# Optimization experiments

Hardware: AMD Instinct MI355X
Metric: run time of the kernel (lower is better)

The kernel has to match this reference:

```python
import jax, jax.numpy as jnp
import numpy as np

N_ENC, B, T, D_ENC = 3, 256, 168, 32
U, H, D_DEC, D_EXT = 256, 24, 1, 16


def _gru_cell(x, h, W, Uw, b):
    # Keras-style GRU cell: gates ordered [z, r, n]; h' = (1-z)*h + z*n
    u = Uw.shape[0]
    xg = x @ W + b            # [B, 3U]
    hg = h @ Uw               # [B, 3U]
    z = jax.nn.sigmoid(xg[:, :u] + hg[:, :u])
    r = jax.nn.sigmoid(xg[:, u:2 * u] + hg[:, u:2 * u])
    n = jnp.tanh(xg[:, 2 * u:] + r * hg[:, 2 * u:])
    return (1.0 - z) * h + z * n


def _run_gru(x, W, Uw, b):
    # x: [B, T, D] -> outputs [B, T, U], last state [B, U]
    h0 = jnp.zeros((x.shape[0], Uw.shape[0]), x.dtype)

    def step(h, xt):
        h2 = _gru_cell(xt, h, W, Uw, b)
        return h2, h2

    hT, ys = jax.lax.scan(step, h0, jnp.swapaxes(x, 0, 1))
    return jnp.swapaxes(ys, 0, 1), hT


def setup_inputs() -> dict:
    key = jax.random.key(0)
    ks = jax.random.split(key, 18)
    s = 0.05
    d_in_dec = N_ENC * U + D_DEC
    d_state = U + N_ENC * U
    return {
        "enc_inputs": jax.random.normal(ks[0], (N_ENC, B, T, D_ENC), jnp.float32),
        "dec_input": jax.random.normal(ks[1], (B, H, D_DEC), jnp.float32),
        "ext_feat": jax.random.normal(ks[2], (B, H, D_EXT), jnp.float32),
        "enc_W": jax.random.normal(ks[3], (N_ENC, D_ENC, 3 * U), jnp.float32) * s,
        "enc_U": jax.random.normal(ks[4], (N_ENC, U, 3 * U), jnp.float32) * s,
        "enc_b": jnp.zeros((N_ENC, 3 * U), jnp.float32),
        "att_W1": jax.random.normal(ks[5], (N_ENC, U, U), jnp.float32) * s,
        "att_W2": jax.random.normal(ks[6], (N_ENC, U, U), jnp.float32) * s,
        "att_v": jax.random.normal(ks[7], (N_ENC, U), jnp.float32) * s,
        "dec_W": jax.random.normal(ks[8], (d_in_dec, 3 * U), jnp.float32) * s,
        "dec_U": jax.random.normal(ks[9], (U, 3 * U), jnp.float32) * s,
        "dec_b": jnp.zeros((3 * U,), jnp.float32),
        "ext_W": jax.random.normal(ks[10], (D_EXT, U), jnp.float32) * s,
        "ext_b": jnp.zeros((U,), jnp.float32),
        "out1_W": jax.random.normal(ks[11], (d_state + U, U), jnp.float32) * s,
        "out1_b": jnp.zeros((U,), jnp.float32),
        "out2_W": jax.random.normal(ks[12], (U, D_DEC), jnp.float32) * s,
        "out2_b": jnp.zeros((D_DEC,), jnp.float32),
    }


def reference(enc_inputs, dec_input, ext_feat, enc_W, enc_U, enc_b,
              att_W1, att_W2, att_v, dec_W, dec_U, dec_b,
              ext_W, ext_b, out1_W, out1_b, out2_W, out2_b):
    b = dec_input.shape[0]
    horizon = dec_input.shape[1]

    # ---- encoders (vmapped GRU over the n_enc streams) ----
    enc_out, _ = jax.vmap(_run_gru)(enc_inputs, enc_W, enc_U, enc_b)  # [n,B,T,U]
    # Precompute Bahdanau keys once: W1 @ enc_outputs
    enc_proj = jnp.einsum('nbtu,nuv->nbtv', enc_out, att_W1)          # [n,B,T,U]

    h0 = jnp.zeros((b, U), dec_input.dtype)
    c0 = jnp.zeros((b, N_ENC * U), dec_input.dtype)

    def dec_step(carry, d_t):
        h, c = carry
        x_t = jnp.concatenate([c, d_t], axis=-1)                      # [B, n*U + D_dec]
        h = _gru_cell(x_t, h, dec_W, dec_U, dec_b)                    # [B, U]
        # Bahdanau attention per encoder, query = decoder state
        q = jnp.einsum('bu,nuv->nbv', h, att_W2)                      # [n,B,U]
        score = jnp.einsum('nbtv,nv->nbt',
                           jnp.tanh(enc_proj + q[:, :, None, :]), att_v)
        alpha = jax.nn.softmax(score, axis=-1)                        # [n,B,T]
        ctx = jnp.einsum('nbt,nbtu->nbu', alpha, enc_out)             # [n,B,U]
        c = jnp.transpose(ctx, (1, 0, 2)).reshape(b, N_ENC * U)
        return (h, c), h

    (h_last, c_last), _ = jax.lax.scan(dec_step, (h0, c0),
                                       jnp.swapaxes(dec_input, 0, 1))

    # ---- output head ----
    state = jnp.concatenate([h_last, c_last], axis=-1)                # [B, U + n*U]
    ed = jnp.broadcast_to(state[:, None, :], (b, horizon, state.shape[-1]))
    ext = jax.nn.relu(ext_feat @ ext_W + ext_b)                       # [B, H, U]
    x = jnp.concatenate([ed, ext], axis=-1)
    x = jax.nn.relu(x @ out1_W + out1_b)
    return x @ out2_W + out2_b                                        # [B, H, target_dim]
```

## Files before the change

kernel.cpp:

```cpp
#include <hip/hip_runtime.h>
#include <math.h>

typedef unsigned short u16;
typedef float f4v __attribute__((ext_vector_type(4)));
typedef _Float16 hfv8 __attribute__((ext_vector_type(8)));

#define MFMAH(a,b,c) __builtin_amdgcn_mfma_f32_16x16x32_f16((a),(b),(c),0,0,0)

__device__ __forceinline__ float bf2f(u16 x){
    unsigned int u = ((unsigned int)x) << 16;
    float f; __builtin_memcpy(&f, &u, 4); return f;
}
__device__ __forceinline__ u16 f2bf(float f){
    unsigned int u; __builtin_memcpy(&u, &f, 4);
    u += 0x7fffu + ((u >> 16) & 1u);
    return (u16)(u >> 16);
}
__device__ __forceinline__ u16 f2h(float f){
    _Float16 h = (_Float16)f;
    u16 b; __builtin_memcpy(&b, &h, 2); return b;
}
__device__ __forceinline__ float h2f(u16 b){
    _Float16 h; __builtin_memcpy(&h, &b, 2); return (float)h;
}
__device__ __forceinline__ float ldmix(const void* p, long i, int mode){
    if (mode) return ((const float*)p)[i];
    return bf2f(((const u16*)p)[i]);
}
__device__ __forceinline__ float frcp(float x){ return __builtin_amdgcn_rcpf(x); }
__device__ __forceinline__ float sigf(float x){ return frcp(1.0f+__expf(-x)); }
__device__ __forceinline__ float tanh_fast(float x){
    float e = __expf(2.0f*x);
    return 1.0f - 2.0f*frcp(1.0f+e);
}

#define BATCH 256
#define TLEN 168
#define HOR 24

#define OFF_FLAG 0ull
#define OFF_SENT 16ull
#define OFF_CNT  128ull
#define OFF_WF   256ull
#define OFF_UP   8721920ull
#define OFF_WP   9901568ull
#define OFF_DWP  10049024ull
#define OFF_DUP  11228672ull
#define OFF_H0   11621888ull
#define OFF_H1   11884032ull
#define OFF_C    12146176ull
#define OFF_W1P  12932608ull
#define OFF_SP   13719040ull
#define OFF_E    13981184ull
#define OFF_PACK0 OFF_E
#define OFF_PACK1 (OFF_E + 524288ull)
#define OFF_W2P   (OFF_E + 1048576ull)
#define OFF_ENCOUT 17126912ull
#define OFF_PROJ 83187200ull
#define NEED_BYTES 149247488ull

#define W_ENCW 0
#define W_ENCU 73728
#define W_ENCB 663552
#define W_AW1  665856
#define W_AW2  862464
#define W_AV   1059072
#define W_DECW 1059840
#define W_DECU 1650432
#define W_DECB 1847040
#define W_EXTW 1847808
#define W_EXTB 1851904
#define W_O1W  1852160
#define W_O1B  2179840
#define W_O2W  2180096
#define W_O2B  2180352

__device__ const int c_wsz[15]  = {73728,589824,2304,196608,196608,768,590592,196608,768,4096,256,327680,256,256,1};
__device__ const int c_woff[15] = {W_ENCW,W_ENCU,W_ENCB,W_AW1,W_AW2,W_AV,W_DECW,W_DECU,W_DECB,W_EXTW,W_EXTB,W_O1W,W_O1B,W_O2W,W_O2B};

struct P15 { const void* p[15]; };

#define SENT_MAGIC 0x5AFE0000u
__device__ __forceinline__ void put_sent(char* ws, int idx){
    ((unsigned int*)(ws+OFF_SENT))[idx] = SENT_MAGIC | (unsigned int)idx;
}

__global__ __launch_bounds__(256) void k_probe(const u16* w16, char* ws)
{
    __shared__ float red[256];
    int tid = threadIdx.x;
    float mb = 0.0f;
    for (int i = tid; i < 2048; i += 256){
        float a = fabsf(bf2f(w16[i]));
        if (a > mb) mb = a;
    }
    red[tid] = mb;
    __syncthreads();
    if (tid == 0){
        for (int i = 1; i < 256; ++i) if (red[i] > mb) mb = red[i];
        *(int*)(ws+OFF_FLAG) = (mb > 1000.0f) ? 1 : 0;
        put_sent(ws, 0);
    }
}

__global__ __launch_bounds__(256) void k_convert(P15 in, char* ws)
{
    int mode = *(const int*)(ws+OFF_FLAG);
    float* F = (float*)(ws+OFF_WF);
    int y = blockIdx.y;
    int sz = c_wsz[y], off = c_woff[y];
    for (long i = (long)blockIdx.x*256 + threadIdx.x; i < sz; i += 256L*256L)
        F[off + i] = ldmix(in.p[y], i, mode);
    if (blockIdx.x==0 && blockIdx.y==0 && threadIdx.x==0) put_sent(ws, 1);
}

__global__ __launch_bounds__(64) void k_pack(char* ws)
{
    const float* F = (const float*)(ws+OFF_WF);
    int m = blockIdx.y;
    if (m >= 11){
        const float* s = F + W_AW2 + (m-11)*65536;
        u16* d = (u16*)(ws+OFF_W2P) + (m-11)*65536;
        int i = blockIdx.x*64 + threadIdx.x;
        if (i < 65536){
            int k = i>>8, u = i&255;
            d[(k>>1)*512 + u*2 + (k&1)] = f2h(s[i]);
        }
        return;
    }
    const float* src; u16* dst; int K, N; int duo = 0;
    switch (m) {
      case 0: case 1: case 2:
        src = F + W_ENCU + m*196608; dst = (u16*)(ws+OFF_UP) + m*196608; K=256; N=768; break;
      case 3: case 4: case 5:
        src = F + W_ENCW + (m-3)*24576; dst = (u16*)(ws+OFF_WP) + (m-3)*24576; K=32; N=768; break;
      case 6:
        src = F + W_DECW; dst = (u16*)(ws+OFF_DWP); K=768; N=768; break;
      case 7:
        src = F + W_DECU; dst = (u16*)(ws+OFF_DUP); K=256; N=768; break;
      default:
        src = F + W_AW1 + (m-8)*65536; dst = (u16*)(ws+OFF_W1P) + (m-8)*131072; K=256; N=256; duo=1; break;
    }
    int KT = K>>5, NT = N>>4;
    int tau = blockIdx.x;
    if (tau < KT*NT){
        int ct = tau / KT, kt = tau % KT;
        int l = threadIdx.x, q = l>>4, c = l&15;
        #pragma unroll
        for (int j = 0; j < 8; ++j){
            float v = src[(size_t)(kt*32 + q*8 + j)*N + ct*16 + c];
            u16 hi = f2h(v);
            size_t di = ((size_t)(ct*KT+kt)*64 + l)*8 + j;
            dst[di] = hi;
            if (duo) dst[65536 + di] = f2h(v - h2f(hi));
        }
    }
    if (blockIdx.x==0 && blockIdx.y==0 && threadIdx.x==0) put_sent(ws, 6);
}

__global__ __launch_bounds__(256) void k_init(char* ws)
{
    long idx = (long)blockIdx.x*256 + threadIdx.x;
    if (idx < 65536) ((float*)(ws+OFF_H0))[idx] = 0.0f;
    else if (idx < 262144) ((float*)(ws+OFF_C))[idx-65536] = 0.0f;
    else if (idx < 393216) ((int*)(ws+OFF_PACK0))[idx-262144] = 0;
    if (idx < 32) ((unsigned*)(ws+OFF_CNT))[idx] = 0u;
}

__global__ __launch_bounds__(512, 2) void k_enc(const void* __restrict__ enc_in,
                                                char* __restrict__ ws,
                                                u16* __restrict__ enc_out)
{
    const float* __restrict__ F = (const float*)(ws+OFF_WF);
    int mode = *(const int*)(ws+OFF_FLAG);
    const int n  = blockIdx.y;
    const int b0 = blockIdx.x*16;
    const int tid = threadIdx.x;
    const int w = tid>>6, l = tid&63, quad = l>>4, c15 = l&15;

    __shared__ __align__(16) u16 hA[2][8][64][8];
    __shared__ __align__(16) u16 sx[2][64][8];
    __shared__ __align__(16) u16 nU[128][64][8];

    const u16* __restrict__ upn = (const u16*)(ws+OFF_UP) + n*196608;
    const u16* __restrict__ wpn = (const u16*)(ws+OFF_WP) + n*24576;

    {
        const uint4* s4 = (const uint4*)(upn + 131072);
        uint4* d4 = (uint4*)&nU[0][0][0];
        for (int i = tid; i < 8192; i += 512) d4[i] = s4[i];
    }
    {
        int* z0 = (int*)&hA[0][0][0][0];
        for (int i = tid; i < 2048; i += 512) z0[i]=0;
    }
    float h[8];
    #pragma unroll
    for (int i=0;i<8;++i) h[i]=0.0f;

    float bzr[2], brr[2], bnr[2];
    #pragma unroll
    for (int si=0;si<2;++si){
        int u = (w*2+si)*16 + c15;
        bzr[si] = F[W_ENCB + n*768 + u];
        brr[si] = F[W_ENCB + n*768 + 256 + u];
        bnr[si] = F[W_ENCB + n*768 + 512 + u];
    }

    hfv8 Bz[2][8], Br[2][8];
    #pragma unroll
    for (int si=0;si<2;++si){
        int ct = w*2+si;
        #pragma unroll
        for (int kt=0;kt<8;++kt){
            Bz[si][kt] = *(const hfv8*)(upn + ((size_t)(ct*8+kt)*64 + l)*8);
            Br[si][kt] = *(const hfv8*)(upn + ((size_t)((16+ct)*8+kt)*64 + l)*8);
        }
    }
    #pragma unroll
    for (int si=0;si<2;++si)
        #pragma unroll
        for (int kt=0;kt<8;++kt)
            asm volatile("" : "+v"(Bz[si][kt]), "+v"(Br[si][kt]));

    const int mm = tid>>5, kk2 = tid&31;
    sx[0][(kk2>>3)*16 + mm][kk2&7] =
        f2h(ldmix(enc_in, (((long)(n*BATCH + b0 + mm))*TLEN + 0)*32 + kk2, mode));
    __syncthreads();

    for (int t = 0; t < TLEN; ++t){
        int p = t & 1;
        int tt = (t+1 < TLEN) ? (t+1) : t;
        float xr = ldmix(enc_in, (((long)(n*BATCH + b0 + mm))*TLEN + tt)*32 + kk2, mode);

        hfv8 ah[8];
        #pragma unroll
        for (int kt=0; kt<8; ++kt)
            ah[kt] = *(const hfv8*)&hA[p][kt][l][0];
        hfv8 ax = *(const hfv8*)&sx[p][l][0];

        #pragma unroll
        for (int si=0; si<2; ++si){
            int ct = w*2 + si;
            f4v az  = {0.f,0.f,0.f,0.f};
            f4v ar  = {0.f,0.f,0.f,0.f};
            f4v anx = {0.f,0.f,0.f,0.f};
            f4v anh = {0.f,0.f,0.f,0.f};
            az  = MFMAH(ax, *(const hfv8*)(wpn + ((size_t)ct*64 + l)*8), az);
            ar  = MFMAH(ax, *(const hfv8*)(wpn + ((size_t)(16+ct)*64 + l)*8), ar);
            anx = MFMAH(ax, *(const hfv8*)(wpn + ((size_t)(32+ct)*64 + l)*8), anx);
            #pragma unroll
            for (int kt=0; kt<8; ++kt) az = MFMAH(ah[kt], Bz[si][kt], az);
            #pragma unroll
            for (int kt=0; kt<8; ++kt) ar = MFMAH(ah[kt], Br[si][kt], ar);
            #pragma unroll
            for (int kt=0; kt<8; ++kt)
                anh = MFMAH(ah[kt], *(const hfv8*)&nU[ct*8+kt][l][0], anh);
            int u = ct*16 + c15;
            #pragma unroll
            for (int j=0;j<4;++j){
                int m = quad*4 + j;
                float z = sigf(az[j] + bzr[si]);
                float r = sigf(ar[j] + brr[si]);
                float ng = tanh_fast(anx[j] + bnr[si] + r*anh[j]);
                float hn = (1.0f - z)*h[si*4+j] + z*ng;
                h[si*4+j] = hn;
                int kt = u>>5, q2 = (u>>3)&3, j2 = u&7;
                hA[1-p][kt][q2*16+m][j2] = f2h(hn);
            }
        }
        sx[1-p][(kk2>>3)*16 + mm][kk2&7] = f2h(xr);
        __syncthreads();
        {
            int c = tid & 31, m2 = tid >> 5;
            *reinterpret_cast<uint4*>(enc_out + (((long)(n*BATCH + b0 + m2))*TLEN + t)*256 + c*8) =
                *(const uint4*)&hA[1-p][c>>2][(c&3)*16 + m2][0];
        }
    }
    if (blockIdx.x==0 && blockIdx.y==0 && tid==0) put_sent(ws, 2);
}

__global__ __launch_bounds__(256) void k_projm(char* __restrict__ ws)
{
    const u16* __restrict__ enc16 = (const u16*)(ws+OFF_ENCOUT);
    const u16* __restrict__ w1p = (const u16*)(ws+OFF_W1P);
    u16* __restrict__ proj = (u16*)(ws+OFF_PROJ);
    const int n = blockIdx.y;
    const long r0 = (long)blockIdx.x*64;
    const int tid = threadIdx.x;
    const int w = tid>>6, l = tid&63, quad = l>>4, c15 = l&15;

    __shared__ __align__(16) u16 ob[64][264];

    const u16* erow = enc16 + ((long)n*43008 + r0 + w*16 + c15)*256;
    hfv8 a[8];
    #pragma unroll
    for (int kt=0; kt<8; ++kt)
        a[kt] = *(const hfv8*)(erow + kt*32 + quad*8);

    const u16* wb = w1p + (long)n*131072;
    #pragma unroll
    for (int ct=0; ct<16; ++ct){
        f4v acc = {0.f,0.f,0.f,0.f};
        #pragma unroll
        for (int kt=0; kt<8; ++kt)
            acc = MFMAH(a[kt], *(const hfv8*)(wb + ((size_t)(ct*8+kt)*64 + l)*8), acc);
        #pragma unroll
        for (int kt=0; kt<8; ++kt)
            acc = MFMAH(a[kt], *(const hfv8*)(wb + 65536 + ((size_t)(ct*8+kt)*64 + l)*8), acc);
        #pragma unroll
        for (int j=0;j<4;++j)
            ob[w*16 + quad*4 + j][ct*16 + c15] = f2h(acc[j]);
    }
    __syncthreads();
    for (int i = tid; i < 2048; i += 256){
        int r = i>>5, c = i&31;
        *reinterpret_cast<uint4*>(proj + ((long)n*43008 + r0 + r)*256 + c*8) =
            *(const uint4*)&ob[r][c*8];
    }
    if (blockIdx.x==0 && blockIdx.y==0 && tid==0) put_sent(ws, 3);
}

__global__ __launch_bounds__(192) void k_dec_gru(
    char* __restrict__ ws, const float* __restrict__ h_in, float* __restrict__ h_out,
    const u16* __restrict__ packC, u16* __restrict__ packN,
    const void* __restrict__ dec_in, int step)
{
    const float* __restrict__ F = (const float*)(ws+OFF_WF);
    int mode = *(const int*)(ws+OFF_FLAG);
    const u16* __restrict__ dwp = (const u16*)(ws+OFF_DWP);
    const u16* __restrict__ dup = (const u16*)(ws+OFF_DUP);
    const int bx = blockIdx.x;
    const int b0 = bx*16;
    const int us = blockIdx.y;
    const int u0 = us*16;
    const int tid = threadIdx.x;
    const int gate = tid>>6, l = tid&63, quad = l>>4, c15 = l&15;
    const int ct = gate*16 + us;

    __shared__ float gz[16][16], gr[16][16], gx[16][16], gh[16][16];

    const u16* pA = packC + (size_t)bx*16384;

    f4v accA  = {0.f,0.f,0.f,0.f};
    f4v accA2 = {0.f,0.f,0.f,0.f};
    f4v accB  = {0.f,0.f,0.f,0.f};
    f4v accB2 = {0.f,0.f,0.f,0.f};

    #pragma unroll
    for (int kg = 0; kg < 32; ++kg){
        hfv8 av = *(const hfv8*)(pA + ((size_t)kg*64 + l)*8);
        const u16* bp = (kg < 24) ? dwp + ((size_t)(ct*24 + kg)*64 + l)*8
                                  : dup + ((size_t)(ct*8  + (kg-24))*64 + l)*8;
        hfv8 bv = *(const hfv8*)bp;
        if (gate == 2 && kg >= 24){
            if (kg & 1) accB2 = MFMAH(av, bv, accB2);
            else        accB  = MFMAH(av, bv, accB);
        } else {
            if (kg & 1) accA2 = MFMAH(av, bv, accA2);
            else        accA  = MFMAH(av, bv, accA);
        }
    }
    accA = accA + accA2;
    accB = accB + accB2;

    #pragma unroll
    for (int j=0;j<4;++j){
        int m = quad*4 + j;
        if (gate == 0) gz[m][c15] = accA[j];
        else if (gate == 1) gr[m][c15] = accA[j];
        else { gx[m][c15] = accA[j]; gh[m][c15] = accB[j]; }
    }
    __syncthreads();
    for (int e = tid; e < 256; e += 192){
        int m = e>>4, j = e&15;
        int u = u0 + j;
        int b = b0 + m;
        float db = ldmix(dec_in, (long)b*HOR + step, mode);
        float sz = gz[m][j] + db*F[W_DECW + 768*768 + u]       + F[W_DECB + u];
        float sr = gr[m][j] + db*F[W_DECW + 768*768 + 256 + u] + F[W_DECB + 256 + u];
        float sn = gx[m][j] + db*F[W_DECW + 768*768 + 512 + u] + F[W_DECB + 512 + u];
        float z = sigf(sz);
        float r = sigf(sr);
        float ng = tanh_fast(sn + r*gh[m][j]);
        float hn = (1.0f - z)*h_in[(long)b*256 + u] + z*ng;
        h_out[(long)b*256 + u] = hn;
        int kk = u & 31;
        int kg = 24 + (u >> 5);
        packN[(((size_t)bx*32 + kg)*64 + (kk>>3)*16 + m)*8 + (kk&7)] = f2h(hn);
    }
}

__global__ __launch_bounds__(512) void k_attn(char* __restrict__ ws,
                                              const float* __restrict__ hvec,
                                              u16* __restrict__ packN)
{
    const float* __restrict__ F = (const float*)(ws+OFF_WF);
    const u16* __restrict__ proj = (const u16*)(ws+OFF_PROJ);
    const u16* __restrict__ enc16 = (const u16*)(ws+OFF_ENCOUT);
    float* __restrict__ C = (float*)(ws+OFF_C);
    const int b = blockIdx.x, n = blockIdx.y;
    const int tid = threadIdx.x;
    const int w = tid>>6, l = tid&63;

    __shared__ float ps[TLEN][65];
    __shared__ float sc[TLEN];
    __shared__ float red[16];
    __shared__ float hrow[256];
    __shared__ float sq[256];
    __shared__ float sqp[2][256];
    __shared__ float ctxp[2][256];

    if (tid < 256) hrow[tid] = hvec[(long)b*256 + tid];
    __syncthreads();

    {
        const u16* W2p = (const u16*)(ws+OFF_W2P) + n*65536;
        int uu = tid & 255, half = tid >> 8;
        float q0=0.f,q1=0.f,q2=0.f,q3=0.f;
        #pragma unroll 4
        for (int k2 = half*64; k2 < half*64+64; k2 += 2){
            unsigned va = *(const unsigned*)(W2p + (size_t)k2*512 + uu*2);
            unsigned vb = *(const unsigned*)(W2p + (size_t)(k2+1)*512 + uu*2);
            q0 += hrow[2*k2  ]*h2f((u16)(va & 0xffffu));
            q1 += hrow[2*k2+1]*h2f((u16)(va >> 16));
            q2 += hrow[2*k2+2]*h2f((u16)(vb & 0xffffu));
            q3 += hrow[2*k2+3]*h2f((u16)(vb >> 16));
        }
        sqp[half][uu] = (q0+q1)+(q2+q3);
    }
    __syncthreads();
    if (tid < 256) sq[tid] = sqp[0][tid] + sqp[1][tid];
    __syncthreads();

    float qv[4], vv[4];
    #pragma unroll
    for (int c4 = 0; c4 < 4; ++c4){
        qv[c4] = sq[c4*64 + l];
        vv[c4] = F[W_AV + n*256 + c4*64 + l];
    }
    long base = ((long)n*43008 + (long)b*TLEN)*256;
    const u16* pb = proj + base;

    for (int i = 0; i < 21; ++i){
        int t = w*21 + i;
        float s = 0.0f;
        #pragma unroll
        for (int c4 = 0; c4 < 4; ++c4){
            float pv = h2f(pb[(long)t*256 + c4*64 + l]);
            s += vv[c4]*tanh_fast(pv + qv[c4]);
        }
        ps[t][l] = s;
    }
    __syncthreads();

    float sval = 0.0f;
    if (tid < TLEN){
        float s0=0.f,s1=0.f,s2=0.f,s3=0.f,s4=0.f,s5=0.f,s6=0.f,s7=0.f;
        #pragma unroll
        for (int j = 0; j < 64; j += 8){
            s0 += ps[tid][j];   s1 += ps[tid][j+1];
            s2 += ps[tid][j+2]; s3 += ps[tid][j+3];
            s4 += ps[tid][j+4]; s5 += ps[tid][j+5];
            s6 += ps[tid][j+6]; s7 += ps[tid][j+7];
        }
        sval = ((s0+s1)+(s2+s3)) + ((s4+s5)+(s6+s7));
    }

    float m = (tid < TLEN) ? sval : -1e30f;
    #pragma unroll
    for (int off = 32; off > 0; off >>= 1) m = fmaxf(m, __shfl_xor(m, off, 64));
    if (l == 0) red[w] = m;
    __syncthreads();
    float mx = fmaxf(fmaxf(fmaxf(red[0],red[1]), fmaxf(red[2],red[3])),
                     fmaxf(fmaxf(red[4],red[5]), fmaxf(red[6],red[7])));

    float ex = 0.0f;
    if (tid < TLEN){ ex = __expf(sval - mx); sc[tid] = ex; }
    float su = ex;
    #pragma unroll
    for (int off = 32; off > 0; off >>= 1) su += __shfl_xor(su, off, 64);
    if (l == 0) red[8+w] = su;
    __syncthreads();
    float inv = frcp(((red[8]+red[9])+(red[10]+red[11])) +
                     ((red[12]+red[13])+(red[14]+red[15])));

    {
        const u16* eb = enc16 + base;
        int uu = tid & 255, half = tid >> 8;
        int t0 = half ? 88 : 0;
        int t1 = half ? 168 : 88;
        float a0=0.f,a1=0.f,a2=0.f,a3=0.f,a4=0.f,a5=0.f,a6=0.f,a7=0.f;
        for (int t = t0; t < t1; t += 8){
            a0 += sc[t  ]*h2f(eb[(long)(t  )*256 + uu]);
            a1 += sc[t+1]*h2f(eb[(long)(t+1)*256 + uu]);
            a2 += sc[t+2]*h2f(eb[(long)(t+2)*256 + uu]);
            a3 += sc[t+3]*h2f(eb[(long)(t+3)*256 + uu]);
            a4 += sc[t+4]*h2f(eb[(long)(t+4)*256 + uu]);
            a5 += sc[t+5]*h2f(eb[(long)(t+5)*256 + uu]);
            a6 += sc[t+6]*h2f(eb[(long)(t+6)*256 + uu]);
            a7 += sc[t+7]*h2f(eb[(long)(t+7)*256 + uu]);
        }
        ctxp[half][uu] = (((a0+a1)+(a2+a3)) + ((a4+a5)+(a6+a7)));
    }
    __syncthreads();
    if (tid < 256){
        float cv = (ctxp[0][tid] + ctxp[1][tid])*inv;
        C[(long)b*768 + n*256 + tid] = cv;
        int kg = n*8 + (tid>>5), kk = tid&31;
        packN[(((size_t)(b>>4)*32 + kg)*64 + (kk>>3)*16 + (b&15))*8 + (kk&7)] = f2h(cv);
    }
    if (b==0 && n==0 && tid==0) put_sent(ws, 4);
}

__global__ __launch_bounds__(256) void k_head1(char* ws, const float* h_last)
{
    const float* F = (const float*)(ws+OFF_WF);
    const float* C = (const float*)(ws+OFF_C);
    float* SP = (float*)(ws+OFF_SP);
    const int b0 = blockIdx.x*8;
    const int tid = threadIdx.x;

    __shared__ float A[8][1024];
    for (int i = tid; i < 8192; i += 256){
        int r = i >> 10, k = i & 1023;
        A[r][k] = (k < 256) ? h_last[(long)(b0+r)*256 + k]
                            : C[(long)(b0+r)*768 + (k-256)];
    }
    __syncthreads();

    const float* W = F + W_O1W;
    float acc[8];
    float bc = F[W_O1B + tid];
    #pragma unroll
    for (int r = 0; r < 8; ++r) acc[r] = bc;
    for (int k = 0; k < 1024; ++k){
        float w = W[k*256 + tid];
        #pragma unroll
        for (int r = 0; r < 8; ++r) acc[r] += A[r][k]*w;
    }
    for (int r = 0; r < 8; ++r)
        SP[(long)(b0+r)*256 + tid] = acc[r];
}

__global__ __launch_bounds__(256) void k_ext(const void* ext_feat, char* ws)
{
    const float* F = (const float*)(ws+OFF_WF);
    u16* E = (u16*)(ws+OFF_E);
    int mode = *(const int*)(ws+OFF_FLAG);
    const int r0 = blockIdx.x*64;
    const int tid = threadIdx.x;
    __shared__ float ef[64][16];
    for (int i = tid; i < 1024; i += 256)
        ef[i>>4][i&15] = ldmix(ext_feat, (long)(r0 + (i>>4))*16 + (i&15), mode);
    float wreg[16];
    #pragma unroll
    for (int k = 0; k < 16; ++k) wreg[k] = F[W_EXTW + k*256 + tid];
    float bb = F[W_EXTB + tid];
    __syncthreads();
    for (int r = 0; r < 64; ++r){
        float a = bb;
        #pragma unroll
        for (int k = 0; k < 16; ++k) a += ef[r][k]*wreg[k];
        E[(long)(r0+r)*256 + tid] = f2bf((a > 0.0f) ? a : 0.0f);
    }
}

__global__ __launch_bounds__(256) void k_head2(char* ws, void* out)
{
    const float* F = (const float*)(ws+OFF_WF);
    const u16* E = (const u16*)(ws+OFF_E);
    const float* SP = (const float*)(ws+OFF_SP);
    int mode = *(const int*)(ws+OFF_FLAG);
    const int r0 = blockIdx.x*16;
    const int tid = threadIdx.x;
    const int w = tid>>6, l = tid&63;

    __shared__ float A[16][256];
    __shared__ float x1[16][257];
    for (int i = tid; i < 4096; i += 256)
        A[i>>8][i&255] = bf2f(E[(long)r0*256 + i]);
    __syncthreads();

    const float* W = F + W_O1W + 1024*256;
    float acc[16];
    float bc = F[W_O1B + tid];
    #pragma unroll
    for (int r = 0; r < 16; ++r) acc[r] = 0.0f;
    for (int k = 0; k < 256; ++k){
        float wv = W[k*256 + tid];
        #pragma unroll
        for (int r = 0; r < 16; ++r) acc[r] += A[r][k]*wv;
    }
    for (int r = 0; r < 16; ++r){
        int g = r0 + r;
        int b = g / HOR;
        float v = acc[r] + SP[(long)b*256 + tid] + bc;
        x1[r][tid] = (v > 0.0f) ? v : 0.0f;
    }
    __syncthreads();

    float w2v[4];
    #pragma unroll
    for (int c4 = 0; c4 < 4; ++c4) w2v[c4] = F[W_O2W + c4*64 + l];
    float b2 = F[W_O2B];
    #pragma unroll
    for (int rr = 0; rr < 4; ++rr){
        int m = w*4 + rr;
        float s = 0.0f;
        #pragma unroll
        for (int c4 = 0; c4 < 4; ++c4) s += x1[m][c4*64 + l]*w2v[c4];
        for (int off = 32; off > 0; off >>= 1) s += __shfl_xor(s, off, 64);
        if (l == 0){
            float val = s + b2;
            long g = r0 + m;
            if (mode == 0) ((u16*)out)[g] = f2bf(val);
            else           ((float*)out)[g] = val;
        }
    }
    if (blockIdx.x==0 && tid==0) put_sent(ws, 5);
}

__global__ __launch_bounds__(64) void MTANet_7593502179851_kernel(char* ws, void* out)
{
    if (threadIdx.x == 0){
        const unsigned int* sent = (const unsigned int*)(ws+OFF_SENT);
        int mode = *(const int*)(ws+OFF_FLAG);
        for (int i = 0; i < 7; ++i){
            if (sent[i] != (SENT_MAGIC | (unsigned int)i)){
                float code = 400.0f + 10.0f*(float)i;
                if (mode == 0) ((u16*)out)[0] = f2bf(code);
                else           ((float*)out)[0] = code;
                break;
            }
        }
    }
}

__global__ __launch_bounds__(64) void k_diag(void* out, float code)
{
    if (threadIdx.x == 0){
        ((u16*)out)[0] = f2bf(code);
        ((float*)out)[1] = code;
    }
}

extern "C" void kernel_launch(void* const* d_in, const int* in_sizes, int n_in,
                              void* d_out, int out_size, void* d_ws, size_t ws_size,
                              hipStream_t stream)
{
    char* ws = (char*)d_ws;

    static const int exp_sizes[18] = {
        4128768, 6144, 98304, 73728, 589824, 2304, 196608, 196608, 768,
        590592, 196608, 768, 4096, 256, 327680, 256, 256, 1 };
    int bad_i = -1;
    if (n_in != 18) bad_i = 99;
    else for (int i = 0; i < 18; ++i)
        if (in_sizes[i] != exp_sizes[i]){ bad_i = i; break; }
    if (bad_i >= 0){
        k_diag<<<dim3(1), dim3(64), 0, stream>>>(d_out, 900.0f + (float)bad_i);
        return;
    }
    if (ws_size < (size_t)NEED_BYTES){
        k_diag<<<dim3(1), dim3(64), 0, stream>>>(d_out, 600.0f);
        return;
    }

    P15 wp;
    for (int i = 0; i < 15; ++i) wp.p[i] = d_in[3+i];

    hipError_t le[12];
    for (int i = 0; i < 12; ++i) le[i] = hipSuccess;
    (void)hipGetLastError();
    #define CHK(slot) { hipError_t e_ = hipGetLastError(); if (e_ != hipSuccess && le[slot] == hipSuccess) le[slot] = e_; }

    k_probe<<<dim3(1), dim3(256), 0, stream>>>((const u16*)d_in[3], ws);       CHK(0)
    k_convert<<<dim3(256,15), dim3(256), 0, stream>>>(wp, ws);                 CHK(1)
    k_pack<<<dim3(1152,14), dim3(64), 0, stream>>>(ws);                        CHK(2)
    k_init<<<dim3(1536), dim3(256), 0, stream>>>(ws);                          CHK(3)
    k_enc<<<dim3(16,3), dim3(512), 0, stream>>>(d_in[0], ws, (u16*)(ws+OFF_ENCOUT)); CHK(4)
    k_projm<<<dim3(672,3), dim3(256), 0, stream>>>(ws);                        CHK(5)

    float* hbuf0 = (float*)(ws+OFF_H0);
    float* hbuf1 = (float*)(ws+OFF_H1);
    u16* pk0 = (u16*)(ws+OFF_PACK0);
    u16* pk1 = (u16*)(ws+OFF_PACK1);
    float* h_last = hbuf0;
    for (int s = 0; s < HOR; ++s){
        float* h_in  = (s & 1) ? hbuf1 : hbuf0;
        float* h_out = (s & 1) ? hbuf0 : hbuf1;
        u16* pc = (s & 1) ? pk1 : pk0;
        u16* pn = (s & 1) ? pk0 : pk1;
        k_dec_gru<<<dim3(16,16), dim3(192), 0, stream>>>(ws, h_in, h_out, pc, pn, d_in[1], s); CHK(6)
        k_attn<<<dim3(256,3), dim3(512), 0, stream>>>(ws, h_out, pn);           CHK(7)
        h_last = h_out;
    }
    k_head1<<<dim3(32), dim3(256), 0, stream>>>(ws, h_last);                   CHK(8)
    k_ext<<<dim3(96), dim3(256), 0, stream>>>(d_in[2], ws);                    CHK(9)
    k_head2<<<dim3(384), dim3(256), 0, stream>>>(ws, d_out);                   CHK(10)
    MTANet_7593502179851_kernel<<<dim3(1), dim3(64), 0, stream>>>(ws, d_out);
    #undef CHK

    for (int i = 0; i < 12; ++i){
        if (le[i] != hipSuccess){
            k_diag<<<dim3(1), dim3(64), 0, stream>>>(d_out, 800.0f + (float)i);
            break;
        }
    }
}
```

Measured before the change: 1.517 ms.

## Halve encoder block size and hold all recurrent GRU weights in registers

The encoder GRU kernel now runs 256 threads per block instead of 512, so each wave handles four 16-column tiles instead of two. The candidate-gate recurrent weights move from shared memory into registers next to the z and r weights, which removes the per-step LDS reads of the n-gate weights. Input staging and output writes loop twice per thread to cover the same data. This greatly raises register pressure (96 hfv8 weight registers per thread) and halves the waves per block, risking spills and less latency hiding in the serial 168-step loop.

Result: slower. 1.934 ms (+27.5%).

```diff
diff --git a/kernel.cpp b/kernel.cpp
--- a/kernel.cpp
+++ b/kernel.cpp
@@ -167,7 +167,7 @@
     if (idx < 32) ((unsigned*)(ws+OFF_CNT))[idx] = 0u;
 }
 
-__global__ __launch_bounds__(512, 2) void k_enc(const void* __restrict__ enc_in,
+__global__ __launch_bounds__(256, 1) void k_enc(const void* __restrict__ enc_in,
                                                 char* __restrict__ ws,
                                                 u16* __restrict__ enc_out)
 {
@@ -180,58 +180,62 @@
 
     __shared__ __align__(16) u16 hA[2][8][64][8];
     __shared__ __align__(16) u16 sx[2][64][8];
-    __shared__ __align__(16) u16 nU[128][64][8];
 
     const u16* __restrict__ upn = (const u16*)(ws+OFF_UP) + n*196608;
     const u16* __restrict__ wpn = (const u16*)(ws+OFF_WP) + n*24576;
 
     {
-        const uint4* s4 = (const uint4*)(upn + 131072);
-        uint4* d4 = (uint4*)&nU[0][0][0];
-        for (int i = tid; i < 8192; i += 512) d4[i] = s4[i];
-    }
-    {
         int* z0 = (int*)&hA[0][0][0][0];
-        for (int i = tid; i < 2048; i += 512) z0[i]=0;
-    }
-    float h[8];
-    #pragma unroll
-    for (int i=0;i<8;++i) h[i]=0.0f;
-
-    float bzr[2], brr[2], bnr[2];
-    #pragma unroll
-    for (int si=0;si<2;++si){
-        int u = (w*2+si)*16 + c15;
+        for (int i = tid; i < 2048; i += 256) z0[i]=0;
+    }
+    float h[16];
+    #pragma unroll
+    for (int i=0;i<16;++i) h[i]=0.0f;
+
+    float bzr[4], brr[4], bnr[4];
+    #pragma unroll
+    for (int si=0;si<4;++si){
+        int u = (w*4+si)*16 + c15;
         bzr[si] = F[W_ENCB + n*768 + u];
         brr[si] = F[W_ENCB + n*768 + 256 + u];
         bnr[si] = F[W_ENCB + n*768 + 512 + u];
     }
 
-    hfv8 Bz[2][8], Br[2][8];
-    #pragma unroll
-    for (int si=0;si<2;++si){
-        int ct = w*2+si;
+    hfv8 Bz[4][8], Br[4][8], Bn[4][8];
+    #pragma unroll
+    for (int si=0;si<4;++si){
+        int ct = w*4+si;
         #pragma unroll
         for (int kt=0;kt<8;++kt){
             Bz[si][kt] = *(const hfv8*)(upn + ((size_t)(ct*8+kt)*64 + l)*8);
             Br[si][kt] = *(const hfv8*)(upn + ((size_t)((16+ct)*8+kt)*64 + l)*8);
-        }
-    }
-    #pragma unroll
-    for (int si=0;si<2;++si)
+            Bn[si][kt] = *(const hfv8*)(upn + ((size_t)((32+ct)*8+kt)*64 + l)*8);
+        }
+    }
+    #pragma unroll
+    for (int si=0;si<4;++si)
         #pragma unroll
         for (int kt=0;kt<8;++kt)
-            asm volatile("" : "+v"(Bz[si][kt]), "+v"(Br[si][kt]));
-
-    const int mm = tid>>5, kk2 = tid&31;
-    sx[0][(kk2>>3)*16 + mm][kk2&7] =
-        f2h(ldmix(enc_in, (((long)(n*BATCH + b0 + mm))*TLEN + 0)*32 + kk2, mode));
+            asm volatile("" : "+v"(Bz[si][kt]), "+v"(Br[si][kt]), "+v"(Bn[si][kt]));
+
+    #pragma unroll
+    for (int rep=0; rep<2; ++rep){
+        int idx = tid + rep*256;
+        int mm = idx>>5, kk2 = idx&31;
+        sx[0][(kk2>>3)*16 + mm][kk2&7] =
+            f2h(ldmix(enc_in, (((long)(n*BATCH + b0 + mm))*TLEN + 0)*32 + kk2, mode));
+    }
     __syncthreads();
 
     for (int t = 0; t < TLEN; ++t){
         int p = t & 1;
         int tt = (t+1 < TLEN) ? (t+1) : t;
-        float xr = ldmix(enc_in, (((long)(n*BATCH + b0 + mm))*TLEN + tt)*32 + kk2, mode);
+        float xr0, xr1;
+        {
+            int idx0 = tid, idx1 = tid + 256;
+            xr0 = ldmix(enc_in, (((long)(n*BATCH + b0 + (idx0>>5)))*TLEN + tt)*32 + (idx0&31), mode);
+            xr1 = ldmix(enc_in, (((long)(n*BATCH + b0 + (idx1>>5)))*TLEN + tt)*32 + (idx1&31), mode);
+        }
 
         hfv8 ah[8];
         #pragma unroll
@@ -240,8 +244,8 @@
         hfv8 ax = *(const hfv8*)&sx[p][l][0];
 
         #pragma unroll
-        for (int si=0; si<2; ++si){
-            int ct = w*2 + si;
+        for (int si=0; si<4; ++si){
+            int ct = w*4 + si;
             f4v az  = {0.f,0.f,0.f,0.f};
             f4v ar  = {0.f,0.f,0.f,0.f};
             f4v anx = {0.f,0.f,0.f,0.f};
@@ -254,8 +258,7 @@
             #pragma unroll
             for (int kt=0; kt<8; ++kt) ar = MFMAH(ah[kt], Br[si][kt], ar);
             #pragma unroll
-            for (int kt=0; kt<8; ++kt)
-                anh = MFMAH(ah[kt], *(const hfv8*)&nU[ct*8+kt][l][0], anh);
+            for (int kt=0; kt<8; ++kt) anh = MFMAH(ah[kt], Bn[si][kt], anh);
             int u = ct*16 + c15;
             #pragma unroll
             for (int j=0;j<4;++j){
@@ -269,10 +272,16 @@
                 hA[1-p][kt][q2*16+m][j2] = f2h(hn);
             }
         }
-        sx[1-p][(kk2>>3)*16 + mm][kk2&7] = f2h(xr);
+        {
+            int idx0 = tid, idx1 = tid + 256;
+            sx[1-p][((idx0&31)>>3)*16 + (idx0>>5)][idx0&7] = f2h(xr0);
+            sx[1-p][((idx1&31)>>3)*16 + (idx1>>5)][idx1&7] = f2h(xr1);
+        }
         __syncthreads();
-        {
-            int c = tid & 31, m2 = tid >> 5;
+        #pragma unroll
+        for (int rep=0; rep<2; ++rep){
+            int idx = tid + rep*256;
+            int c = idx & 31, m2 = idx >> 5;
             *reinterpret_cast<uint4*>(enc_out + (((long)(n*BATCH + b0 + m2))*TLEN + t)*256 + c*8) =
                 *(const uint4*)&hA[1-p][c>>2][(c&3)*16 + m2][0];
         }
@@ -679,7 +688,7 @@
     k_convert<<<dim3(256,15), dim3(256), 0, stream>>>(wp, ws);                 CHK(1)
     k_pack<<<dim3(1152,14), dim3(64), 0, stream>>>(ws);                        CHK(2)
     k_init<<<dim3(1536), dim3(256), 0, stream>>>(ws);                          CHK(3)
-    k_enc<<<dim3(16,3), dim3(512), 0, stream>>>(d_in[0], ws, (u16*)(ws+OFF_ENCOUT)); CHK(4)
+    k_enc<<<dim3(16,3), dim3(256), 0, stream>>>(d_in[0], ws, (u16*)(ws+OFF_ENCOUT)); CHK(4)
     k_projm<<<dim3(672,3), dim3(256), 0, stream>>>(ws);                        CHK(5)
 
     float* hbuf0 = (float*)(ws+OFF_H0);
```
